# Kernel tuning notes

Hardware: AMD Instinct MI355X
Metric: run time of the kernel (lower is better)

## Reference

```python
import jax, jax.numpy as jnp
import numpy as np

D_MODEL = 1024
D_INNER = 2048
N_EXPERTS = 8
TOP_K = 2
INIT_STD = 0.02


def setup_inputs() -> dict:
    key = jax.random.key(0)
    ks = jax.random.split(key, 6)
    B, S = 2, 2048
    x = jax.random.normal(ks[0], (B, S, D_MODEL), dtype=jnp.float32)
    router_w = jax.random.normal(ks[1], (N_EXPERTS, D_MODEL), dtype=jnp.float32) * (INIT_STD * 0.1)
    router_b = jnp.zeros((N_EXPERTS,), dtype=jnp.float32)
    gate_w = jax.random.normal(ks[2], (N_EXPERTS, D_MODEL, D_INNER), dtype=jnp.float32) * INIT_STD
    up_w = jax.random.normal(ks[3], (N_EXPERTS, D_MODEL, D_INNER), dtype=jnp.float32) * INIT_STD
    down_w = jax.random.normal(ks[4], (N_EXPERTS, D_INNER, D_MODEL), dtype=jnp.float32) * INIT_STD
    return {"x": x, "router_w": router_w, "router_b": router_b,
            "gate_w": gate_w, "up_w": up_w, "down_w": down_w}


def reference(x, router_w, router_b, gate_w, up_w, down_w):
    # Router: softmax over experts, top-k, renormalize top-k probs.
    logits = jnp.einsum('bsd,ed->bse', x, router_w) + router_b          # [B,S,E]
    probs = jax.nn.softmax(logits, axis=-1)
    top_p, top_i = jax.lax.top_k(probs, TOP_K)                           # [B,S,K]
    top_p = top_p / jnp.sum(top_p, axis=-1, keepdims=True)
    # Per-expert combine weight: c[b,s,e] = sum_k top_p[b,s,k] * [top_i[b,s,k]==e]
    onehot = jax.nn.one_hot(top_i, N_EXPERTS, dtype=x.dtype)             # [B,S,K,E]
    combine = jnp.einsum('bsk,bske->bse', top_p, onehot)                 # [B,S,E]
    # SwiGLU FFN for every expert (dense form of the masked dispatch),
    # zeroed/weighted by combine coefficients.
    g = jnp.einsum('bsd,edf->ebsf', x, gate_w)                           # [E,B,S,F]
    u = jnp.einsum('bsd,edf->ebsf', x, up_w)
    h = jax.nn.silu(g) * u
    y = jnp.einsum('ebsf,efd->ebsd', h, down_w)                          # [E,B,S,D]
    out = jnp.einsum('ebsd,bse->bsd', y, combine)
    return out
```

## Files before the change

### kernel.cpp

```cpp
#include <hip/hip_runtime.h>
#include <hip/hip_bf16.h>
#include <stdint.h>

#define D_MODEL 1024
#define D_INNER 2048
#define NEXP 8
#define TOPK 2
#define T256 40
#define T128 72

typedef float f32x4 __attribute__((ext_vector_type(4)));
typedef short bf16x8 __attribute__((ext_vector_type(8)));

#define MEMFENCE asm volatile("" ::: "memory")

__device__ __forceinline__ unsigned short f2b(float f) {
    union { float f; uint32_t u; } v; v.f = f;
    uint32_t u = v.u;
    return (unsigned short)((u + 0x7fffu + ((u >> 16) & 1u)) >> 16);
}

__device__ __forceinline__ void gl_lds16(const void* g, void* l) {
    __builtin_amdgcn_global_load_lds((const __attribute__((address_space(1))) void*)g,
                                     (__attribute__((address_space(3))) void*)l, 16, 0, 0);
}

__global__ __launch_bounds__(256) void tcast3_kernel(
    const float* __restrict__ gw, const float* __restrict__ uw, const float* __restrict__ dw,
    unsigned short* __restrict__ gT, unsigned short* __restrict__ uT, unsigned short* __restrict__ dT)
{
    __shared__ unsigned short S[64][68];
    int which = blockIdx.z >> 3;
    int e = blockIdx.z & 7;
    const float* in; unsigned short* out; int K, N;
    if (which == 0)      { in = gw; out = gT; K = D_MODEL; N = D_INNER; }
    else if (which == 1) { in = uw; out = uT; K = D_MODEL; N = D_INNER; }
    else                 { in = dw; out = dT; K = D_INNER; N = D_MODEL; }
    int n0 = blockIdx.x * 64, k0 = blockIdx.y * 64;
    if (n0 >= N || k0 >= K) return;
    const float* ib = in + (size_t)e * K * N;
    unsigned short* ob = out + (size_t)e * N * K;
    int tid = threadIdx.x;
    int kk = tid >> 4, nn4 = (tid & 15) * 4;
#pragma unroll
    for (int j = 0; j < 4; j++) {
        int k = kk + 16 * j;
        float4 v = *(const float4*)&ib[(size_t)(k0 + k) * N + n0 + nn4];
        ushort4 s; s.x = f2b(v.x); s.y = f2b(v.y); s.z = f2b(v.z); s.w = f2b(v.w);
        *(ushort4*)&S[k][nn4] = s;
    }
    __syncthreads();
    int nn = tid >> 4, kk4 = (tid & 15) * 4;
#pragma unroll
    for (int j = 0; j < 4; j++) {
        int n = nn + 16 * j;
        ushort4 s;
        s.x = S[kk4 + 0][n]; s.y = S[kk4 + 1][n];
        s.z = S[kk4 + 2][n]; s.w = S[kk4 + 3][n];
        *(ushort4*)&ob[(size_t)(n0 + n) * K + k0 + kk4] = s;
    }
}

__global__ __launch_bounds__(64) void router_kernel(
    const float* __restrict__ x, const float* __restrict__ rw,
    const float* __restrict__ rb, unsigned short* __restrict__ xb,
    int* __restrict__ top_i, float* __restrict__ top_w, int T)
{
    int t = blockIdx.x;
    if (t >= T) return;
    int l = threadIdx.x;
    float xv[16];
#pragma unroll
    for (int i = 0; i < 16; i++) xv[i] = x[(size_t)t * D_MODEL + l + 64 * i];
#pragma unroll
    for (int i = 0; i < 16; i++) xb[(size_t)t * D_MODEL + l + 64 * i] = f2b(xv[i]);
    float logit[NEXP];
#pragma unroll
    for (int e = 0; e < NEXP; e++) {
        float acc = 0.f;
#pragma unroll
        for (int i = 0; i < 16; i++) acc += xv[i] * rw[e * D_MODEL + l + 64 * i];
#pragma unroll
        for (int s = 32; s > 0; s >>= 1) acc += __shfl_xor(acc, s, 64);
        logit[e] = acc + rb[e];
    }
    if (l == 0) {
        int i0 = 0; float m0 = logit[0];
#pragma unroll
        for (int e = 1; e < NEXP; e++) if (logit[e] > m0) { m0 = logit[e]; i0 = e; }
        int i1 = -1; float m1 = -3.0e38f;
#pragma unroll
        for (int e = 0; e < NEXP; e++) {
            if (e == i0) continue;
            if (logit[e] > m1) { m1 = logit[e]; i1 = e; }
        }
        float w0 = 1.f / (1.f + expf(m1 - m0));
        top_i[t * 2 + 0] = i0; top_i[t * 2 + 1] = i1;
        top_w[t * 2 + 0] = w0; top_w[t * 2 + 1] = 1.f - w0;
    }
}

__global__ __launch_bounds__(256) void bucket_kernel(
    const int* __restrict__ top_i, const float* __restrict__ top_w,
    int* __restrict__ meta, int* __restrict__ tok_of_slot,
    float* __restrict__ w_of_slot, int T)
{
    __shared__ int cnt[256][NEXP];
    __shared__ int pre[256][NEXP];
    __shared__ int tot[NEXP];
    __shared__ int off[NEXP + 1];
    int tid = threadIdx.x;
    int per = (T + 255) / 256;
    int t0 = tid * per;
    for (int e = 0; e < NEXP; e++) cnt[tid][e] = 0;
    for (int t = t0; t < t0 + per && t < T; t++)
        for (int k = 0; k < TOPK; k++) cnt[tid][top_i[t * 2 + k]]++;
    __syncthreads();
    if (tid < NEXP) {
        int run = 0;
        for (int i = 0; i < 256; i++) { pre[i][tid] = run; run += cnt[i][tid]; }
        tot[tid] = run;
    }
    __syncthreads();
    if (tid == 0) {
        off[0] = 0;
        for (int e = 0; e < NEXP; e++) off[e + 1] = off[e] + tot[e];
        for (int e = 0; e <= NEXP; e++) meta[e] = off[e];
        int nt = 0;
        for (int e = 0; e < NEXP; e++)
            for (int r = off[e]; r < off[e + 1]; r += 256)
                meta[16 + nt++] = (e << 16) | r;
        meta[11] = nt;
        for (; nt < T256; nt++) meta[16 + nt] = -1;
        nt = 0;
        for (int e = 0; e < NEXP; e++)
            for (int r = off[e]; r < off[e + 1]; r += 128)
                meta[64 + nt++] = (e << 16) | r;
        meta[12] = nt;
        for (; nt < T128; nt++) meta[64 + nt] = -1;
    }
    __syncthreads();
    int lc[NEXP];
#pragma unroll
    for (int e = 0; e < NEXP; e++) lc[e] = 0;
    for (int t = t0; t < t0 + per && t < T; t++) {
        for (int k = 0; k < TOPK; k++) {
            int e = top_i[t * 2 + k];
            int slot = off[e] + pre[tid][e] + lc[e]++;
            tok_of_slot[slot] = t;
            w_of_slot[slot] = top_w[t * 2 + k];
        }
    }
}

__global__ __launch_bounds__(512, 1) void moe_gate_up(
    const unsigned short* __restrict__ xb, const unsigned short* __restrict__ wgT,
    const unsigned short* __restrict__ wuT, const int* __restrict__ meta,
    const int* __restrict__ tok_of_slot, unsigned short* __restrict__ H,
    int* __restrict__ ctr)
{
    extern __shared__ __align__(16) unsigned short lds[];
    __shared__ int sm_wid;

    int tid = threadIdx.x, wv = tid >> 6, lane = tid & 63;
    int c = tid & 7, rr = tid >> 3;
    int wm = wv >> 1, wn = wv & 1;
    int lrow = lane & 15, kgrp = lane >> 4;
    int sw = lrow & 7;
    int co0 = 8 * (kgrp ^ sw);
    int co1 = 8 * ((4 + kgrp) ^ sw);
    int arow[4], brow[4];
#pragma unroll
    for (int i = 0; i < 4; i++) arow[i] = (wm * 64 + i * 16 + lrow) * 64;
#pragma unroll
    for (int i = 0; i < 4; i++) brow[i] = (wn * 64 + i * 16 + lrow) * 64;

    int n256 = meta[11];
    int nwork = n256 * 16;

    for (;;) {
        __syncthreads();
        if (tid == 0) sm_wid = atomicAdd(ctr, 1);
        __syncthreads();
        int wid = sm_wid;
        if (wid >= nwork) break;
        int strip = wid / n256, tix = wid - strip * n256;
        int packed = meta[16 + tix];
        int e = packed >> 16, row0 = packed & 0xffff;
        int Mloc = min(256, meta[e + 1] - row0);
        int f0 = strip * 128;

        const unsigned short* srcA[4];
        const unsigned short* srcG[2];
        const unsigned short* srcU[2];
#pragma unroll
        for (int j = 0; j < 4; j++) {
            int row = j * 64 + rr;
            int slot = row0 + ((row < Mloc) ? row : 0);
            srcA[j] = xb + (size_t)tok_of_slot[slot] * D_MODEL + 8 * (c ^ (row & 7));
        }
#pragma unroll
        for (int j = 0; j < 2; j++) {
            int row = j * 64 + rr;
            size_t wb = (size_t)e * D_MODEL * D_INNER + (size_t)(f0 + row) * D_MODEL + 8 * (c ^ (row & 7));
            srcG[j] = wgT + wb; srcU[j] = wuT + wb;
        }

        f32x4 accg[4][4], accu[4][4];
#pragma unroll
        for (int i = 0; i < 4; i++)
#pragma unroll
            for (int j = 0; j < 4; j++) {
                accg[i][j] = (f32x4){0.f, 0.f, 0.f, 0.f};
                accu[i][j] = (f32x4){0.f, 0.f, 0.f, 0.f};
            }

        auto stage = [&](int u) {
            int kk = u * 64;
            unsigned short* base = lds + (u & 1) * 32768;
#pragma unroll
            for (int j = 0; j < 4; j++)
                gl_lds16(srcA[j] + kk, base + (j * 512 + wv * 64) * 8);
#pragma unroll
            for (int j = 0; j < 2; j++) {
                gl_lds16(srcG[j] + kk, base + 16384 + (j * 512 + wv * 64) * 8);
                gl_lds16(srcU[j] + kk, base + 24576 + (j * 512 + wv * 64) * 8);
            }
        };

        bf16x8 a[4], bg[4], bu[4];
        auto load_frags = [&](int u, int co) {
            const unsigned short* base = lds + (u & 1) * 32768;
#pragma unroll
            for (int i = 0; i < 4; i++) a[i] = *(const bf16x8*)(base + arow[i] + co);
#pragma unroll
            for (int i = 0; i < 4; i++) bg[i] = *(const bf16x8*)(base + 16384 + brow[i] + co);
#pragma unroll
            for (int i = 0; i < 4; i++) bu[i] = *(const bf16x8*)(base + 24576 + brow[i] + co);
        };

        const int NT = D_MODEL / 64;
        stage(0);
        MEMFENCE;
        asm volatile("s_waitcnt vmcnt(0)" ::: "memory");
        __builtin_amdgcn_s_barrier();
        MEMFENCE;
        load_frags(0, co0);

        for (int t = 0; t < NT; ++t) {
            if (t + 1 < NT) stage(t + 1);
            __builtin_amdgcn_sched_barrier(0);
            __builtin_amdgcn_s_setprio(1);
#pragma unroll
            for (int fm = 0; fm < 4; fm++)
#pragma unroll
                for (int fn = 0; fn < 4; fn++) {
                    accg[fm][fn] = __builtin_amdgcn_mfma_f32_16x16x32_bf16(a[fm], bg[fn], accg[fm][fn], 0, 0, 0);
                    accu[fm][fn] = __builtin_amdgcn_mfma_f32_16x16x32_bf16(a[fm], bu[fn], accu[fm][fn], 0, 0, 0);
                }
            __builtin_amdgcn_s_setprio(0);
            load_frags(t, co1);
            __builtin_amdgcn_s_setprio(1);
#pragma unroll
            for (int fm = 0; fm < 4; fm++)
#pragma unroll
                for (int fn = 0; fn < 4; fn++) {
                    accg[fm][fn] = __builtin_amdgcn_mfma_f32_16x16x32_bf16(a[fm], bg[fn], accg[fm][fn], 0, 0, 0);
                    accu[fm][fn] = __builtin_amdgcn_mfma_f32_16x16x32_bf16(a[fm], bu[fn], accu[fm][fn], 0, 0, 0);
                }
            __builtin_amdgcn_s_setprio(0);
            __builtin_amdgcn_sched_barrier(0);
            asm volatile("s_waitcnt vmcnt(0)" ::: "memory");
            __builtin_amdgcn_s_barrier();
            MEMFENCE;
            if (t + 1 < NT) load_frags(t + 1, co0);
        }

#pragma unroll
        for (int fm = 0; fm < 4; fm++)
#pragma unroll
            for (int fn = 0; fn < 4; fn++)
#pragma unroll
                for (int r = 0; r < 4; r++) {
                    int m = wm * 64 + fm * 16 + kgrp * 4 + r;
                    if (m < Mloc) {
                        int n = wn * 64 + fn * 16 + lrow;
                        float g = accg[fm][fn][r], u = accu[fm][fn][r];
                        float h = g / (1.f + __expf(-g)) * u;
                        H[(size_t)(row0 + m) * D_INNER + f0 + n] = f2b(h);
                    }
                }
    }
}

__global__ __launch_bounds__(512, 1) void moe_down(
    const unsigned short* __restrict__ H, const unsigned short* __restrict__ wdT,
    const int* __restrict__ meta, const int* __restrict__ tok_of_slot,
    const float* __restrict__ w_of_slot, float* __restrict__ out, int S2,
    int* __restrict__ ctr)
{
    extern __shared__ __align__(16) unsigned short lds[];
    __shared__ int toks[128];
    __shared__ float wts[128];
    __shared__ int sm_wid;

    int tid = threadIdx.x, wv = tid >> 6, lane = tid & 63;
    int c = tid & 7, rr = tid >> 3;
    int wm = wv >> 2, wn = wv & 3;
    int lrow = lane & 15, kgrp = lane >> 4;
    int sw = lrow & 7;
    int co0 = 8 * (kgrp ^ sw);
    int co1 = 8 * ((4 + kgrp) ^ sw);
    int arow[4], brow[4];
#pragma unroll
    for (int i = 0; i < 4; i++) arow[i] = (wm * 64 + i * 16 + lrow) * 64;
#pragma unroll
    for (int i = 0; i < 4; i++) brow[i] = 8192 + (wn * 64 + i * 16 + lrow) * 64;

    int n128 = meta[12];
    int nwork = n128 * 4;

    for (;;) {
        __syncthreads();
        if (tid == 0) sm_wid = atomicAdd(ctr, 1);
        __syncthreads();
        int wid = sm_wid;
        if (wid >= nwork) break;
        int dstrip = wid / n128, tix = wid - dstrip * n128;
        int packed = meta[64 + tix];
        int e = packed >> 16, row0 = packed & 0xffff;
        int Mloc = min(128, meta[e + 1] - row0);
        int d0 = dstrip * 256;

        if (tid < 128) {
            bool v = tid < Mloc;
            toks[tid] = v ? tok_of_slot[row0 + tid] : 0;
            wts[tid] = v ? w_of_slot[row0 + tid] : 0.f;
        }

        const unsigned short* srcA[2];
        const unsigned short* srcB[4];
#pragma unroll
        for (int j = 0; j < 2; j++) {
            int row = j * 64 + rr;
            int slot = min(row0 + row, S2 - 1);
            srcA[j] = H + (size_t)slot * D_INNER + 8 * (c ^ (row & 7));
        }
#pragma unroll
        for (int j = 0; j < 4; j++) {
            int row = j * 64 + rr;
            srcB[j] = wdT + (size_t)e * D_INNER * D_MODEL + (size_t)(d0 + row) * D_INNER + 8 * (c ^ (row & 7));
        }

        f32x4 acc[4][4];
#pragma unroll
        for (int i = 0; i < 4; i++)
#pragma unroll
            for (int j = 0; j < 4; j++) acc[i][j] = (f32x4){0.f, 0.f, 0.f, 0.f};

        auto stage = [&](int u) {
            int kk = u * 64;
            unsigned short* base = lds + (u & 1) * 24576;
#pragma unroll
            for (int j = 0; j < 2; j++)
                gl_lds16(srcA[j] + kk, base + (j * 512 + wv * 64) * 8);
#pragma unroll
            for (int j = 0; j < 4; j++)
                gl_lds16(srcB[j] + kk, base + 8192 + (j * 512 + wv * 64) * 8);
        };

        bf16x8 a[4], b[4];
        auto load_frags = [&](int u, int co) {
            const unsigned short* base = lds + (u & 1) * 24576;
#pragma unroll
            for (int i = 0; i < 4; i++) a[i] = *(const bf16x8*)(base + arow[i] + co);
#pragma unroll
            for (int i = 0; i < 4; i++) b[i] = *(const bf16x8*)(base + brow[i] + co);
        };

        const int NT = D_INNER / 64;
        stage(0);
        MEMFENCE;
        asm volatile("s_waitcnt vmcnt(0)" ::: "memory");
        __builtin_amdgcn_s_barrier();
        MEMFENCE;
        load_frags(0, co0);

        for (int t = 0; t < NT; ++t) {
            if (t + 1 < NT) stage(t + 1);
            __builtin_amdgcn_sched_barrier(0);
            __builtin_amdgcn_s_setprio(1);
#pragma unroll
            for (int fm = 0; fm < 4; fm++)
#pragma unroll
                for (int fn = 0; fn < 4; fn++)
                    acc[fm][fn] = __builtin_amdgcn_mfma_f32_16x16x32_bf16(a[fm], b[fn], acc[fm][fn], 0, 0, 0);
            __builtin_amdgcn_s_setprio(0);
            load_frags(t, co1);
            __builtin_amdgcn_s_setprio(1);
#pragma unroll
            for (int fm = 0; fm < 4; fm++)
#pragma unroll
                for (int fn = 0; fn < 4; fn++)
                    acc[fm][fn] = __builtin_amdgcn_mfma_f32_16x16x32_bf16(a[fm], b[fn], acc[fm][fn], 0, 0, 0);
            __builtin_amdgcn_s_setprio(0);
            __builtin_amdgcn_sched_barrier(0);
            asm volatile("s_waitcnt vmcnt(0)" ::: "memory");
            __builtin_amdgcn_s_barrier();
            MEMFENCE;
            if (t + 1 < NT) load_frags(t + 1, co0);
        }

#pragma unroll
        for (int fm = 0; fm < 4; fm++)
#pragma unroll
            for (int fn = 0; fn < 4; fn++)
#pragma unroll
                for (int r = 0; r < 4; r++) {
                    int m = wm * 64 + fm * 16 + kgrp * 4 + r;
                    if (m < Mloc) {
                        int n = d0 + wn * 64 + fn * 16 + lrow;
                        atomicAdd(&out[(size_t)toks[m] * D_MODEL + n], wts[m] * acc[fm][fn][r]);
                    }
                }
    }
}

extern "C" void kernel_launch(void* const* d_in, const int* in_sizes, int n_in,
                              void* d_out, int out_size, void* d_ws, size_t ws_size,
                              hipStream_t stream) {
    const float* x  = (const float*)d_in[0];
    const float* rw = (const float*)d_in[1];
    const float* rb = (const float*)d_in[2];
    const float* gw = (const float*)d_in[3];
    const float* uw = (const float*)d_in[4];
    const float* dw = (const float*)d_in[5];
    float* out = (float*)d_out;

    int T = in_sizes[0] / D_MODEL;
    int S2 = 2 * T;

    char* ws = (char*)d_ws;
    size_t cur = 0;
    auto take = [&](size_t bytes) { char* p = ws + cur; cur = (cur + bytes + 255) & ~(size_t)255; return p; };
    int*   ctrs  = (int*)take(256);
    int*   top_i = (int*)take((size_t)S2 * 4);
    float* top_w = (float*)take((size_t)S2 * 4);
    int*   meta  = (int*)take(1024);
    int*   tos   = (int*)take((size_t)S2 * 4);
    float* wos   = (float*)take((size_t)S2 * 4);
    unsigned short* xb  = (unsigned short*)take((size_t)T * D_MODEL * 2);
    unsigned short* wgT = (unsigned short*)take((size_t)NEXP * D_MODEL * D_INNER * 2);
    unsigned short* wuT = (unsigned short*)take((size_t)NEXP * D_MODEL * D_INNER * 2);
    unsigned short* wdT = (unsigned short*)take((size_t)NEXP * D_MODEL * D_INNER * 2);
    unsigned short* H   = (unsigned short*)take((size_t)S2 * D_INNER * 2);

    static const int GU_LDS = 2 * 32768 * 2;
    static const int DN_LDS = 2 * 24576 * 2;
    hipFuncSetAttribute((const void*)moe_gate_up,
                        hipFuncAttributeMaxDynamicSharedMemorySize, GU_LDS);
    hipFuncSetAttribute((const void*)moe_down,
                        hipFuncAttributeMaxDynamicSharedMemorySize, DN_LDS);

    hipMemsetAsync(ctrs, 0, 256, stream);
    hipMemsetAsync(d_out, 0, (size_t)out_size * sizeof(float), stream);

    tcast3_kernel<<<dim3(32, 32, 24), 256, 0, stream>>>(gw, uw, dw, wgT, wuT, wdT);
    router_kernel<<<T, 64, 0, stream>>>(x, rw, rb, xb, top_i, top_w, T);
    bucket_kernel<<<1, 256, 0, stream>>>(top_i, top_w, meta, tos, wos, T);

    moe_gate_up<<<256, 512, GU_LDS, stream>>>(xb, wgT, wuT, meta, tos, H, &ctrs[0]);
    moe_down<<<256, 512, DN_LDS, stream>>>(H, wdT, meta, tos, wos, out, S2, &ctrs[1]);
}
```

Baseline: 275.0 us.

## Restructure MoE GEMM main loops into phased ping-pong schedule with triple-buffered down

```diff
diff --git a/kernel.cpp b/kernel.cpp
--- a/kernel.cpp
+++ b/kernel.cpp
@@ -13,6 +13,11 @@
 typedef short bf16x8 __attribute__((ext_vector_type(8)));
 
 #define MEMFENCE asm volatile("" ::: "memory")
+#define SB __builtin_amdgcn_sched_barrier(0)
+#define LGKM0 asm volatile("s_waitcnt lgkmcnt(0)" ::: "memory")
+#define VM0 asm volatile("s_waitcnt vmcnt(0)" ::: "memory")
+#define VM6 asm volatile("s_waitcnt vmcnt(6)" ::: "memory")
+#define BAR __builtin_amdgcn_s_barrier()
 
 __device__ __forceinline__ unsigned short f2b(float f) {
     union { float f; uint32_t u; } v; v.f = f;
@@ -163,17 +168,20 @@
     __shared__ int sm_wid;
 
     int tid = threadIdx.x, wv = tid >> 6, lane = tid & 63;
+    int lrow = lane & 15, kgrp = lane >> 4, sw = lrow & 7;
+    int mh = wv >> 2, sel = (wv >> 1) & 1, fh = wv & 1;
     int c = tid & 7, rr = tid >> 3;
-    int wm = wv >> 1, wn = wv & 1;
-    int lrow = lane & 15, kgrp = lane >> 4;
-    int sw = lrow & 7;
+    int cx8 = (c ^ (rr & 7)) * 8;
     int co0 = 8 * (kgrp ^ sw);
     int co1 = 8 * ((4 + kgrp) ^ sw);
-    int arow[4], brow[4];
-#pragma unroll
-    for (int i = 0; i < 4; i++) arow[i] = (wm * 64 + i * 16 + lrow) * 64;
-#pragma unroll
-    for (int i = 0; i < 4; i++) brow[i] = (wn * 64 + i * 16 + lrow) * 64;
+    int dL = wv * 512 + lane * 8;
+
+    int aoff[8], boff[4];
+#pragma unroll
+    for (int i = 0; i < 8; i++) aoff[i] = (mh * 128 + i * 16 + lrow) * 64;
+    int bbase = 16384 + sel * 8192;
+#pragma unroll
+    for (int i = 0; i < 4; i++) boff[i] = bbase + (fh * 64 + i * 16 + lrow) * 64;
 
     int n256 = meta[11];
     int nwork = n256 * 16;
@@ -190,106 +198,156 @@
         int Mloc = min(256, meta[e + 1] - row0);
         int f0 = strip * 128;
 
-        const unsigned short* srcA[4];
-        const unsigned short* srcG[2];
-        const unsigned short* srcU[2];
+        const unsigned short* sA[4];
 #pragma unroll
         for (int j = 0; j < 4; j++) {
             int row = j * 64 + rr;
             int slot = row0 + ((row < Mloc) ? row : 0);
-            srcA[j] = xb + (size_t)tok_of_slot[slot] * D_MODEL + 8 * (c ^ (row & 7));
-        }
+            sA[j] = xb + (size_t)tok_of_slot[slot] * D_MODEL + cx8;
+        }
+        const unsigned short *sG[2], *sU[2];
 #pragma unroll
         for (int j = 0; j < 2; j++) {
             int row = j * 64 + rr;
-            size_t wb = (size_t)e * D_MODEL * D_INNER + (size_t)(f0 + row) * D_MODEL + 8 * (c ^ (row & 7));
-            srcG[j] = wgT + wb; srcU[j] = wuT + wb;
-        }
-
-        f32x4 accg[4][4], accu[4][4];
-#pragma unroll
-        for (int i = 0; i < 4; i++)
-#pragma unroll
-            for (int j = 0; j < 4; j++) {
-                accg[i][j] = (f32x4){0.f, 0.f, 0.f, 0.f};
-                accu[i][j] = (f32x4){0.f, 0.f, 0.f, 0.f};
-            }
-
-        auto stage = [&](int u) {
-            int kk = u * 64;
-            unsigned short* base = lds + (u & 1) * 32768;
-#pragma unroll
-            for (int j = 0; j < 4; j++)
-                gl_lds16(srcA[j] + kk, base + (j * 512 + wv * 64) * 8);
+            size_t wb = (size_t)e * D_MODEL * D_INNER + (size_t)(f0 + row) * D_MODEL + cx8;
+            sG[j] = wgT + wb; sU[j] = wuT + wb;
+        }
+
+        f32x4 acc[8][4];
+#pragma unroll
+        for (int i = 0; i < 8; i++)
+#pragma unroll
+            for (int j = 0; j < 4; j++) acc[i][j] = (f32x4){0.f, 0.f, 0.f, 0.f};
+
+        {
+            unsigned short* b = lds;
+#pragma unroll
+            for (int j = 0; j < 4; j++) gl_lds16(sA[j], b + j * 4096 + dL);
 #pragma unroll
             for (int j = 0; j < 2; j++) {
-                gl_lds16(srcG[j] + kk, base + 16384 + (j * 512 + wv * 64) * 8);
-                gl_lds16(srcU[j] + kk, base + 24576 + (j * 512 + wv * 64) * 8);
-            }
-        };
-
-        bf16x8 a[4], bg[4], bu[4];
-        auto load_frags = [&](int u, int co) {
-            const unsigned short* base = lds + (u & 1) * 32768;
-#pragma unroll
-            for (int i = 0; i < 4; i++) a[i] = *(const bf16x8*)(base + arow[i] + co);
-#pragma unroll
-            for (int i = 0; i < 4; i++) bg[i] = *(const bf16x8*)(base + 16384 + brow[i] + co);
-#pragma unroll
-            for (int i = 0; i < 4; i++) bu[i] = *(const bf16x8*)(base + 24576 + brow[i] + co);
-        };
-
-        const int NT = D_MODEL / 64;
-        stage(0);
-        MEMFENCE;
-        asm volatile("s_waitcnt vmcnt(0)" ::: "memory");
-        __builtin_amdgcn_s_barrier();
-        MEMFENCE;
-        load_frags(0, co0);
-
-        for (int t = 0; t < NT; ++t) {
-            if (t + 1 < NT) stage(t + 1);
-            __builtin_amdgcn_sched_barrier(0);
+                gl_lds16(sG[j], b + 16384 + j * 4096 + dL);
+                gl_lds16(sU[j], b + 24576 + j * 4096 + dL);
+            }
+        }
+        MEMFENCE; VM0; BAR; MEMFENCE;
+
+        for (int kt = 0; kt < 16; ++kt) {
+            const unsigned short* buf = lds + (kt & 1) * 32768;
+            unsigned short* nb = lds + ((kt + 1) & 1) * 32768;
+            int kk = (kt + 1) * 64;
+            bool pf = (kt + 1) < 16;
+            bf16x8 Aq[4][2], B0[2][2], B1[2][2];
+
+#pragma unroll
+            for (int i = 0; i < 4; i++) {
+                Aq[i][0] = *(const bf16x8*)(buf + aoff[i] + co0);
+                Aq[i][1] = *(const bf16x8*)(buf + aoff[i] + co1);
+            }
+#pragma unroll
+            for (int j = 0; j < 2; j++) {
+                B0[j][0] = *(const bf16x8*)(buf + boff[j] + co0);
+                B0[j][1] = *(const bf16x8*)(buf + boff[j] + co1);
+            }
+            if (pf) {
+                gl_lds16(sA[0] + kk, nb + dL);
+                gl_lds16(sA[1] + kk, nb + 4096 + dL);
+                gl_lds16(sG[0] + kk, nb + 16384 + dL);
+            }
+            SB; BAR; LGKM0; SB;
             __builtin_amdgcn_s_setprio(1);
 #pragma unroll
-            for (int fm = 0; fm < 4; fm++)
-#pragma unroll
-                for (int fn = 0; fn < 4; fn++) {
-                    accg[fm][fn] = __builtin_amdgcn_mfma_f32_16x16x32_bf16(a[fm], bg[fn], accg[fm][fn], 0, 0, 0);
-                    accu[fm][fn] = __builtin_amdgcn_mfma_f32_16x16x32_bf16(a[fm], bu[fn], accu[fm][fn], 0, 0, 0);
+            for (int i = 0; i < 4; i++)
+#pragma unroll
+                for (int j = 0; j < 2; j++) {
+                    acc[i][j] = __builtin_amdgcn_mfma_f32_16x16x32_bf16(Aq[i][0], B0[j][0], acc[i][j], 0, 0, 0);
+                    acc[i][j] = __builtin_amdgcn_mfma_f32_16x16x32_bf16(Aq[i][1], B0[j][1], acc[i][j], 0, 0, 0);
                 }
             __builtin_amdgcn_s_setprio(0);
-            load_frags(t, co1);
+            SB; BAR;
+
+#pragma unroll
+            for (int j = 0; j < 2; j++) {
+                B1[j][0] = *(const bf16x8*)(buf + boff[2 + j] + co0);
+                B1[j][1] = *(const bf16x8*)(buf + boff[2 + j] + co1);
+            }
+            if (pf) {
+                gl_lds16(sA[2] + kk, nb + 8192 + dL);
+                gl_lds16(sA[3] + kk, nb + 12288 + dL);
+                gl_lds16(sU[0] + kk, nb + 24576 + dL);
+            }
+            SB; BAR; LGKM0; SB;
             __builtin_amdgcn_s_setprio(1);
 #pragma unroll
-            for (int fm = 0; fm < 4; fm++)
-#pragma unroll
-                for (int fn = 0; fn < 4; fn++) {
-                    accg[fm][fn] = __builtin_amdgcn_mfma_f32_16x16x32_bf16(a[fm], bg[fn], accg[fm][fn], 0, 0, 0);
-                    accu[fm][fn] = __builtin_amdgcn_mfma_f32_16x16x32_bf16(a[fm], bu[fn], accu[fm][fn], 0, 0, 0);
+            for (int i = 0; i < 4; i++)
+#pragma unroll
+                for (int j = 0; j < 2; j++) {
+                    acc[i][2 + j] = __builtin_amdgcn_mfma_f32_16x16x32_bf16(Aq[i][0], B1[j][0], acc[i][2 + j], 0, 0, 0);
+                    acc[i][2 + j] = __builtin_amdgcn_mfma_f32_16x16x32_bf16(Aq[i][1], B1[j][1], acc[i][2 + j], 0, 0, 0);
                 }
             __builtin_amdgcn_s_setprio(0);
-            __builtin_amdgcn_sched_barrier(0);
-            asm volatile("s_waitcnt vmcnt(0)" ::: "memory");
-            __builtin_amdgcn_s_barrier();
-            MEMFENCE;
-            if (t + 1 < NT) load_frags(t + 1, co0);
-        }
-
-#pragma unroll
-        for (int fm = 0; fm < 4; fm++)
-#pragma unroll
-            for (int fn = 0; fn < 4; fn++)
-#pragma unroll
-                for (int r = 0; r < 4; r++) {
-                    int m = wm * 64 + fm * 16 + kgrp * 4 + r;
-                    if (m < Mloc) {
-                        int n = wn * 64 + fn * 16 + lrow;
-                        float g = accg[fm][fn][r], u = accu[fm][fn][r];
-                        float h = g / (1.f + __expf(-g)) * u;
-                        H[(size_t)(row0 + m) * D_INNER + f0 + n] = f2b(h);
+            SB; BAR;
+
+#pragma unroll
+            for (int i = 0; i < 4; i++) {
+                Aq[i][0] = *(const bf16x8*)(buf + aoff[4 + i] + co0);
+                Aq[i][1] = *(const bf16x8*)(buf + aoff[4 + i] + co1);
+            }
+            if (pf) {
+                gl_lds16(sG[1] + kk, nb + 16384 + 4096 + dL);
+                gl_lds16(sU[1] + kk, nb + 24576 + 4096 + dL);
+            }
+            SB; BAR; LGKM0; SB;
+            __builtin_amdgcn_s_setprio(1);
+#pragma unroll
+            for (int i = 0; i < 4; i++)
+#pragma unroll
+                for (int j = 0; j < 2; j++) {
+                    acc[4 + i][j] = __builtin_amdgcn_mfma_f32_16x16x32_bf16(Aq[i][0], B0[j][0], acc[4 + i][j], 0, 0, 0);
+                    acc[4 + i][j] = __builtin_amdgcn_mfma_f32_16x16x32_bf16(Aq[i][1], B0[j][1], acc[4 + i][j], 0, 0, 0);
+                }
+            __builtin_amdgcn_s_setprio(0);
+            SB; BAR;
+
+            __builtin_amdgcn_s_setprio(1);
+#pragma unroll
+            for (int i = 0; i < 4; i++)
+#pragma unroll
+                for (int j = 0; j < 2; j++) {
+                    acc[4 + i][2 + j] = __builtin_amdgcn_mfma_f32_16x16x32_bf16(Aq[i][0], B1[j][0], acc[4 + i][2 + j], 0, 0, 0);
+                    acc[4 + i][2 + j] = __builtin_amdgcn_mfma_f32_16x16x32_bf16(Aq[i][1], B1[j][1], acc[4 + i][2 + j], 0, 0, 0);
+                }
+            __builtin_amdgcn_s_setprio(0);
+            SB; VM0; BAR; MEMFENCE;
+        }
+
+        float* reg = (float*)lds + (mh * 2 + fh) * 8320;
+        if (sel == 1) {
+#pragma unroll
+            for (int fm = 0; fm < 8; fm++)
+#pragma unroll
+                for (int fn = 0; fn < 4; fn++)
+#pragma unroll
+                    for (int r = 0; r < 4; r++)
+                        reg[(fm * 16 + kgrp * 4 + r) * 65 + fn * 16 + lrow] = acc[fm][fn][r];
+        }
+        __syncthreads();
+        if (sel == 0) {
+#pragma unroll
+            for (int fm = 0; fm < 8; fm++)
+#pragma unroll
+                for (int fn = 0; fn < 4; fn++)
+#pragma unroll
+                    for (int r = 0; r < 4; r++) {
+                        int row = fm * 16 + kgrp * 4 + r;
+                        int m = mh * 128 + row;
+                        if (m < Mloc) {
+                            float g = acc[fm][fn][r];
+                            float u = reg[row * 65 + fn * 16 + lrow];
+                            float h = g / (1.f + __expf(-g)) * u;
+                            H[(size_t)(row0 + m) * D_INNER + f0 + fh * 64 + fn * 16 + lrow] = f2b(h);
+                        }
                     }
-                }
+        }
     }
 }
 
@@ -305,17 +363,19 @@
     __shared__ int sm_wid;
 
     int tid = threadIdx.x, wv = tid >> 6, lane = tid & 63;
+    int lrow = lane & 15, kgrp = lane >> 4, sw = lrow & 7;
+    int mh = wv >> 2, nh = wv & 3;
     int c = tid & 7, rr = tid >> 3;
-    int wm = wv >> 2, wn = wv & 3;
-    int lrow = lane & 15, kgrp = lane >> 4;
-    int sw = lrow & 7;
+    int cx8 = (c ^ (rr & 7)) * 8;
     int co0 = 8 * (kgrp ^ sw);
     int co1 = 8 * ((4 + kgrp) ^ sw);
-    int arow[4], brow[4];
-#pragma unroll
-    for (int i = 0; i < 4; i++) arow[i] = (wm * 64 + i * 16 + lrow) * 64;
-#pragma unroll
-    for (int i = 0; i < 4; i++) brow[i] = 8192 + (wn * 64 + i * 16 + lrow) * 64;
+    int dL = wv * 512 + lane * 8;
+
+    int aoff[4], boff[4];
+#pragma unroll
+    for (int i = 0; i < 4; i++) aoff[i] = (mh * 64 + i * 16 + lrow) * 64;
+#pragma unroll
+    for (int i = 0; i < 4; i++) boff[i] = 8192 + (nh * 64 + i * 16 + lrow) * 64;
 
     int n128 = meta[12];
     int nwork = n128 * 4;
@@ -338,18 +398,18 @@
             wts[tid] = v ? w_of_slot[row0 + tid] : 0.f;
         }
 
-        const unsigned short* srcA[2];
-        const unsigned short* srcB[4];
+        const unsigned short* sA[2];
+        const unsigned short* sBv[4];
 #pragma unroll
         for (int j = 0; j < 2; j++) {
             int row = j * 64 + rr;
             int slot = min(row0 + row, S2 - 1);
-            srcA[j] = H + (size_t)slot * D_INNER + 8 * (c ^ (row & 7));
+            sA[j] = H + (size_t)slot * D_INNER + cx8;
         }
 #pragma unroll
         for (int j = 0; j < 4; j++) {
             int row = j * 64 + rr;
-            srcB[j] = wdT + (size_t)e * D_INNER * D_MODEL + (size_t)(d0 + row) * D_INNER + 8 * (c ^ (row & 7));
+            sBv[j] = wdT + (size_t)e * D_INNER * D_MODEL + (size_t)(d0 + row) * D_INNER + cx8;
         }
 
         f32x4 acc[4][4];
@@ -358,57 +418,74 @@
 #pragma unroll
             for (int j = 0; j < 4; j++) acc[i][j] = (f32x4){0.f, 0.f, 0.f, 0.f};
 
-        auto stage = [&](int u) {
+#pragma unroll
+        for (int u = 0; u < 2; u++) {
+            unsigned short* b = lds + u * 24576;
             int kk = u * 64;
-            unsigned short* base = lds + (u & 1) * 24576;
-#pragma unroll
-            for (int j = 0; j < 2; j++)
-                gl_lds16(srcA[j] + kk, base + (j * 512 + wv * 64) * 8);
-#pragma unroll
-            for (int j = 0; j < 4; j++)
-                gl_lds16(srcB[j] + kk, base + 8192 + (j * 512 + wv * 64) * 8);
-        };
-
-        bf16x8 a[4], b[4];
-        auto load_frags = [&](int u, int co) {
-            const unsigned short* base = lds + (u & 1) * 24576;
-#pragma unroll
-            for (int i = 0; i < 4; i++) a[i] = *(const bf16x8*)(base + arow[i] + co);
-#pragma unroll
-            for (int i = 0; i < 4; i++) b[i] = *(const bf16x8*)(base + brow[i] + co);
-        };
-
-        const int NT = D_INNER / 64;
-        stage(0);
-        MEMFENCE;
-        asm volatile("s_waitcnt vmcnt(0)" ::: "memory");
-        __builtin_amdgcn_s_barrier();
-        MEMFENCE;
-        load_frags(0, co0);
-
-        for (int t = 0; t < NT; ++t) {
-            if (t + 1 < NT) stage(t + 1);
-            __builtin_amdgcn_sched_barrier(0);
+#pragma unroll
+            for (int j = 0; j < 2; j++) gl_lds16(sA[j] + kk, b + j * 4096 + dL);
+#pragma unroll
+            for (int j = 0; j < 4; j++) gl_lds16(sBv[j] + kk, b + 8192 + j * 4096 + dL);
+        }
+        MEMFENCE; VM6; BAR; MEMFENCE;
+
+        for (int kt = 0; kt < 32; ++kt) {
+            const unsigned short* buf = lds + (kt % 3) * 24576;
+            unsigned short* nb = lds + ((kt + 2) % 3) * 24576;
+            int kk = (kt + 2) * 64;
+            bool pf = (kt + 2) < 32;
+            bf16x8 Aq[4][2], B0[2][2], B1[2][2];
+
+#pragma unroll
+            for (int i = 0; i < 4; i++) {
+                Aq[i][0] = *(const bf16x8*)(buf + aoff[i] + co0);
+                Aq[i][1] = *(const bf16x8*)(buf + aoff[i] + co1);
+            }
+#pragma unroll
+            for (int j = 0; j < 2; j++) {
+                B0[j][0] = *(const bf16x8*)(buf + boff[j] + co0);
+                B0[j][1] = *(const bf16x8*)(buf + boff[j] + co1);
+            }
+            if (pf) {
+                gl_lds16(sA[0] + kk, nb + dL);
+                gl_lds16(sA[1] + kk, nb + 4096 + dL);
+                gl_lds16(sBv[0] + kk, nb + 8192 + dL);
+            }
+            SB; BAR; LGKM0; SB;
             __builtin_amdgcn_s_setprio(1);
 #pragma unroll
-            for (int fm = 0; fm < 4; fm++)
-#pragma unroll
-                for (int fn = 0; fn < 4; fn++)
-                    acc[fm][fn] = __builtin_amdgcn_mfma_f32_16x16x32_bf16(a[fm], b[fn], acc[fm][fn], 0, 0, 0);
+            for (int i = 0; i < 4; i++)
+#pragma unroll
+                for (int j = 0; j < 2; j++) {
+                    acc[i][j] = __builtin_amdgcn_mfma_f32_16x16x32_bf16(Aq[i][0], B0[j][0], acc[i][j], 0, 0, 0);
+                    acc[i][j] = __builtin_amdgcn_mfma_f32_16x16x32_bf16(Aq[i][1], B0[j][1], acc[i][j], 0, 0, 0);
+                }
             __builtin_amdgcn_s_setprio(0);
-            load_frags(t, co1);
+            SB; BAR;
+
+#pragma unroll
+            for (int j = 0; j < 2; j++) {
+                B1[j][0] = *(const bf16x8*)(buf + boff[2 + j] + co0);
+                B1[j][1] = *(const bf16x8*)(buf + boff[2 + j] + co1);
+            }
+            if (pf) {
+                gl_lds16(sBv[1] + kk, nb + 8192 + 4096 + dL);
+                gl_lds16(sBv[2] + kk, nb + 8192 + 8192 + dL);
+                gl_lds16(sBv[3] + kk, nb + 8192 + 12288 + dL);
+            }
+            SB; BAR; LGKM0; SB;
             __builtin_amdgcn_s_setprio(1);
 #pragma unroll
-            for (int fm = 0; fm < 4; fm++)
-#pragma unroll
-                for (int fn = 0; fn < 4; fn++)
-                    acc[fm][fn] = __builtin_amdgcn_mfma_f32_16x16x32_bf16(a[fm], b[fn], acc[fm][fn], 0, 0, 0);
+            for (int i = 0; i < 4; i++)
+#pragma unroll
+                for (int j = 0; j < 2; j++) {
+                    acc[i][2 + j] = __builtin_amdgcn_mfma_f32_16x16x32_bf16(Aq[i][0], B1[j][0], acc[i][2 + j], 0, 0, 0);
+                    acc[i][2 + j] = __builtin_amdgcn_mfma_f32_16x16x32_bf16(Aq[i][1], B1[j][1], acc[i][2 + j], 0, 0, 0);
+                }
             __builtin_amdgcn_s_setprio(0);
-            __builtin_amdgcn_sched_barrier(0);
-            asm volatile("s_waitcnt vmcnt(0)" ::: "memory");
-            __builtin_amdgcn_s_barrier();
-            MEMFENCE;
-            if (t + 1 < NT) load_frags(t + 1, co0);
+            SB;
+            if (pf) { VM6; } else { VM0; }
+            BAR; MEMFENCE;
         }
 
 #pragma unroll
@@ -417,9 +494,9 @@
             for (int fn = 0; fn < 4; fn++)
 #pragma unroll
                 for (int r = 0; r < 4; r++) {
-                    int m = wm * 64 + fm * 16 + kgrp * 4 + r;
+                    int m = mh * 64 + fm * 16 + kgrp * 4 + r;
                     if (m < Mloc) {
-                        int n = d0 + wn * 64 + fn * 16 + lrow;
+                        int n = d0 + nh * 64 + fn * 16 + lrow;
                         atomicAdd(&out[(size_t)toks[m] * D_MODEL + n], wts[m] * acc[fm][fn][r]);
                     }
                 }
@@ -455,8 +532,8 @@
     unsigned short* wdT = (unsigned short*)take((size_t)NEXP * D_MODEL * D_INNER * 2);
     unsigned short* H   = (unsigned short*)take((size_t)S2 * D_INNER * 2);
 
-    static const int GU_LDS = 2 * 32768 * 2;
-    static const int DN_LDS = 2 * 24576 * 2;
+    static const int GU_LDS = 133120;
+    static const int DN_LDS = 3 * 24576 * 2;
     hipFuncSetAttribute((const void*)moe_gate_up,
                         hipFuncAttributeMaxDynamicSharedMemorySize, GU_LDS);
     hipFuncSetAttribute((const void*)moe_down,
```

After: 321.0 us. 1.17x slower.
